# Optimization experiments

Hardware: AMD Instinct MI355X
Metric: run time of the kernel (lower is better)

The kernel has to match this reference:

```python
import jax, jax.numpy as jnp
import numpy as np

DIM = 512
GLBL = 108
N = 100000
NUM_SEGMENTS = 1024


def setup_inputs() -> dict:
    key = jax.random.key(0)
    ks = jax.random.split(key, 9)
    x = jax.random.normal(ks[0], (N, DIM), dtype=jnp.float32)
    glbl_x = jax.random.normal(ks[1], (N, GLBL), dtype=jnp.float32)
    batch = jnp.sort(jax.random.randint(ks[2], (N,), 0, NUM_SEGMENTS, dtype=jnp.int32))
    # MLP params: (dim+108 -> dim), (dim -> dim), (dim -> 1)
    s0 = 1.0 / np.sqrt(DIM + GLBL)
    s1 = 1.0 / np.sqrt(DIM)
    W0 = jax.random.uniform(ks[3], (DIM + GLBL, DIM), jnp.float32, -s0, s0)
    b0 = jax.random.uniform(ks[4], (DIM,), jnp.float32, -s0, s0)
    W1 = jax.random.uniform(ks[5], (DIM, DIM), jnp.float32, -s1, s1)
    b1 = jax.random.uniform(ks[6], (DIM,), jnp.float32, -s1, s1)
    W2 = jax.random.uniform(ks[7], (DIM, 1), jnp.float32, -s1, s1)
    b2 = jax.random.uniform(ks[8], (1,), jnp.float32, -s1, s1)
    return {"x": x, "batch": batch, "glbl_x": glbl_x,
            "W0": W0, "b0": b0, "W1": W1, "b1": b1, "W2": W2, "b2": b2}


def segment_softmax(logits, seg, num_segments):
    # logits: [N, 1]; per-segment numerically-stable softmax (torch_geometric softmax)
    m = jax.ops.segment_max(logits, seg, num_segments=num_segments)  # [G, 1]
    e = jnp.exp(logits - m[seg])
    s = jax.ops.segment_sum(e, seg, num_segments=num_segments)       # [G, 1]
    return e / (s[seg] + 1e-16)


def reference(x, batch, glbl_x, W0, b0, W1, b1, W2, b2):
    out = jnp.concatenate([x, glbl_x], axis=-1)          # [N, dim+108]
    out = jax.nn.softplus(out @ W0 + b0)                 # [N, dim]
    out = jax.nn.softplus(out @ W1 + b1)                 # [N, dim]
    out = out @ W2 + b2                                  # [N, 1]
    return segment_softmax(out, batch, NUM_SEGMENTS)     # [N, 1]
```

## Files before the change

kernel.cpp:

```cpp
#include <hip/hip_runtime.h>
#include <hip/hip_bf16.h>
#include <math.h>


#define NSEG 1024

typedef __attribute__((ext_vector_type(8))) short short8;
typedef __attribute__((ext_vector_type(4))) float f32x4;

__device__ __forceinline__ unsigned short f2bf(float f) {
  __hip_bfloat16 h = __float2bfloat16(f);
  return *reinterpret_cast<unsigned short*>(&h);
}
__device__ __forceinline__ float softplus_fast(float z) {
  float t = __expf(-fabsf(z));
  return fmaxf(z, 0.f) + __logf(1.f + t);
}
__device__ __forceinline__ void gll16(const void* g, void* l) {
  __builtin_amdgcn_global_load_lds(
      (const __attribute__((address_space(1))) void*)g,
      (__attribute__((address_space(3))) void*)l, 16, 0, 0);
}
__device__ __forceinline__ int xcd_swz(int bid, int nwg) {
  int q = nwg >> 3, r = nwg & 7, x = bid & 7, i = bid >> 3;
  return (x < r ? x * (q + 1) : r * (q + 1) + (x - r) * q) + i;
}

__global__ __launch_bounds__(256) void prep(const float* __restrict__ W0,
                                            const float* __restrict__ W1,
                                            unsigned short* __restrict__ W0T,
                                            unsigned short* __restrict__ W1T,
                                            float* __restrict__ logits, int Mp) {
  int t = blockIdx.x * 256 + threadIdx.x;
  if (t < 512 * 640) {
    int n = t / 640, k = t % 640;
    W0T[t] = f2bf(k < 620 ? W0[(size_t)k * 512 + n] : 0.f);
    return;
  }
  t -= 512 * 640;
  if (t < 512 * 512) {
    int n = t / 512, k = t % 512;
    W1T[t] = f2bf(W1[(size_t)k * 512 + n]);
    return;
  }
  t -= 512 * 512;
  if (t < Mp) logits[t] = 0.f;
}

__global__ __launch_bounds__(256) void pack_g(const float* __restrict__ gx,
                                              float* __restrict__ G32,
                                              int N, int Mp) {
  int t = blockIdx.x * 256 + threadIdx.x;
  if (t >= Mp * 32) return;
  int row = t >> 5, c = (t & 31) << 2;
  float4 v;
  v.x = (row < N && c + 0 < 108) ? gx[(size_t)row * 108 + c + 0] : 0.f;
  v.y = (row < N && c + 1 < 108) ? gx[(size_t)row * 108 + c + 1] : 0.f;
  v.z = (row < N && c + 2 < 108) ? gx[(size_t)row * 108 + c + 2] : 0.f;
  v.w = (row < N && c + 3 < 108) ? gx[(size_t)row * 108 + c + 3] : 0.f;
  *reinterpret_cast<float4*>(G32 + (size_t)row * 128 + c) = v;
}

__global__ __launch_bounds__(256, 3) void gemm0(const float* __restrict__ x,
                                                const float* __restrict__ G32,
                                                const unsigned short* __restrict__ W0T,
                                                const float* __restrict__ b0,
                                                unsigned short* __restrict__ H0,
                                                int N, int nwg) {
  constexpr int K = 640, KT = 20;
  __shared__ float Asf[2][128 * 32];
  __shared__ unsigned short Ws[2][128 * 32];
  const int L = xcd_swz(blockIdx.x, nwg);
  const int nt = L & 3, mt = L >> 2;
  const int tid = threadIdx.x, lane = tid & 63, wid = tid >> 6;
  const int wm = wid >> 1, wn = wid & 1, lm = lane & 15, rch = lane >> 4;

  const unsigned short* Wg = W0T + (size_t)(nt * 128) * K;

  f32x4 acc[4][4] = {};

  auto stageA = [&](int buf, int kb) {
#pragma unroll
    for (int i2 = 0; i2 < 4; ++i2) {
      int f = i2 * 256 + tid;
      int r = f >> 3, s = f & 7;
      int g4 = (s ^ (r & 7)) << 2;
      const float* src;
      if (kb < 512) {
        int rg = mt * 128 + r; if (rg >= N) rg = N - 1;
        src = x + (size_t)rg * 512 + kb + g4;
      } else {
        int rg = mt * 128 + r;
        src = G32 + (size_t)rg * 128 + (kb - 512) + g4;
      }
      gll16(src, &Asf[buf][r * 32 + s * 4]);
    }
  };
  auto stageW = [&](int buf, int kb) {
#pragma unroll
    for (int i2 = 0; i2 < 2; ++i2) {
      int f = i2 * 256 + tid;
      int row = f >> 2;
      int sc = ((f & 3) ^ ((row >> 1) & 3)) << 3;
      gll16(Wg + (size_t)row * K + kb + sc, &Ws[buf][f * 8]);
    }
  };

  stageA(0, 0);
  stageW(0, 0);

  for (int kt = 0; kt < KT; ++kt) {
    const int cur = kt & 1;
    __syncthreads();
    if (kt + 1 < KT) { stageA(cur ^ 1, (kt + 1) * 32); stageW(cur ^ 1, (kt + 1) * 32); }

    short8 af[4], wf[4];
#pragma unroll
    for (int mi = 0; mi < 4; ++mi) {
      int rw = wm * 64 + mi * 16 + lm;
      const float* base = &Asf[cur][rw * 32];
      f32x4 lo = *reinterpret_cast<const f32x4*>(base + ((((2 * rch) ^ (rw & 7)) << 2)));
      f32x4 hi = *reinterpret_cast<const f32x4*>(base + ((((2 * rch + 1) ^ (rw & 7)) << 2)));
      union { unsigned short u[8]; short8 s8; } cv;
#pragma unroll
      for (int j = 0; j < 4; ++j) { cv.u[j] = f2bf(lo[j]); cv.u[4 + j] = f2bf(hi[j]); }
      af[mi] = cv.s8;
    }
#pragma unroll
    for (int ni = 0; ni < 4; ++ni) {
      int rw = wn * 64 + ni * 16 + lm;
      wf[ni] = *reinterpret_cast<const short8*>(
          &Ws[cur][rw * 32 + ((rch ^ ((rw >> 1) & 3)) << 3)]);
    }
    __builtin_amdgcn_s_setprio(1);
#pragma unroll
    for (int mi = 0; mi < 4; ++mi)
#pragma unroll
      for (int ni = 0; ni < 4; ++ni)
        acc[mi][ni] = __builtin_amdgcn_mfma_f32_16x16x32_bf16(wf[ni], af[mi], acc[mi][ni], 0, 0, 0);
    __builtin_amdgcn_s_setprio(0);
  }

#pragma unroll
  for (int mi = 0; mi < 4; ++mi) {
    const int m = mt * 128 + wm * 64 + mi * 16 + lm;
#pragma unroll
    for (int ni = 0; ni < 4; ++ni) {
      const int n0 = nt * 128 + wn * 64 + ni * 16 + (rch << 2);
      const f32x4 bb = *reinterpret_cast<const f32x4*>(b0 + n0);
      f32x4 v = acc[mi][ni];
      union { unsigned short u[4]; uint2 qv; } o;
#pragma unroll
      for (int rr = 0; rr < 4; ++rr) o.u[rr] = f2bf(softplus_fast(v[rr] + bb[rr]));
      *reinterpret_cast<uint2*>(H0 + (size_t)m * 512 + n0) = o.qv;
    }
  }
}

__global__ __launch_bounds__(256, 4) void gemm1(const unsigned short* __restrict__ H0,
                                                const unsigned short* __restrict__ W1T,
                                                const float* __restrict__ b1,
                                                const float* __restrict__ W2,
                                                float* __restrict__ logits, int nwg) {
  constexpr int K = 512, KT = 16;
  __shared__ unsigned short As[2][128 * 32];
  __shared__ unsigned short Ws[2][128 * 32];
  const int L = xcd_swz(blockIdx.x, nwg);
  const int nt = L & 3, mt = L >> 2;
  const int tid = threadIdx.x, lane = tid & 63, wid = tid >> 6;
  const int wm = wid >> 1, wn = wid & 1, lm = lane & 15, rch = lane >> 4;

  const unsigned short* Ag = H0 + (size_t)(mt * 128) * K;
  const unsigned short* Wg = W1T + (size_t)(nt * 128) * K;

  f32x4 acc[4][4] = {};

  auto stage = [&](int buf, int kb) {
#pragma unroll
    for (int i2 = 0; i2 < 2; ++i2) {
      int f = i2 * 256 + tid;
      int row = f >> 2;
      int sc = ((f & 3) ^ ((row >> 1) & 3)) << 3;
      gll16(Ag + (size_t)row * K + kb + sc, &As[buf][f * 8]);
      gll16(Wg + (size_t)row * K + kb + sc, &Ws[buf][f * 8]);
    }
  };

  stage(0, 0);

  for (int kt = 0; kt < KT; ++kt) {
    const int cur = kt & 1;
    __syncthreads();
    if (kt + 1 < KT) stage(cur ^ 1, (kt + 1) * 32);

    short8 af[4], wf[4];
#pragma unroll
    for (int mi = 0; mi < 4; ++mi) {
      int rw = wm * 64 + mi * 16 + lm;
      af[mi] = *reinterpret_cast<const short8*>(
          &As[cur][rw * 32 + ((rch ^ ((rw >> 1) & 3)) << 3)]);
    }
#pragma unroll
    for (int ni = 0; ni < 4; ++ni) {
      int rw = wn * 64 + ni * 16 + lm;
      wf[ni] = *reinterpret_cast<const short8*>(
          &Ws[cur][rw * 32 + ((rch ^ ((rw >> 1) & 3)) << 3)]);
    }
    __builtin_amdgcn_s_setprio(1);
#pragma unroll
    for (int mi = 0; mi < 4; ++mi)
#pragma unroll
      for (int ni = 0; ni < 4; ++ni)
        acc[mi][ni] = __builtin_amdgcn_mfma_f32_16x16x32_bf16(wf[ni], af[mi], acc[mi][ni], 0, 0, 0);
    __builtin_amdgcn_s_setprio(0);
  }

#pragma unroll
  for (int mi = 0; mi < 4; ++mi) {
    const int m = mt * 128 + wm * 64 + mi * 16 + lm;
    float part = 0.f;
#pragma unroll
    for (int ni = 0; ni < 4; ++ni) {
      const int n0 = nt * 128 + wn * 64 + ni * 16 + (rch << 2);
      const f32x4 bb = *reinterpret_cast<const f32x4*>(b1 + n0);
      const f32x4 wv = *reinterpret_cast<const f32x4*>(W2 + n0);
      f32x4 v = acc[mi][ni];
#pragma unroll
      for (int rr = 0; rr < 4; ++rr) part += softplus_fast(v[rr] + bb[rr]) * wv[rr];
    }
    part += __shfl_xor(part, 16);
    part += __shfl_xor(part, 32);
    if (lane < 16) atomicAdd(logits + m, part);
  }
}

__global__ __launch_bounds__(256) void segsoftmax(const float* __restrict__ logits,
                                                  const int* __restrict__ batch,
                                                  float* __restrict__ out, int N) {
  const int g = blockIdx.x;
  const int tid = threadIdx.x;
  int lo = 0, hi = N;
  while (lo < hi) { int mid = (lo + hi) >> 1; if (batch[mid] < g) lo = mid + 1; else hi = mid; }
  const int beg = lo;
  hi = N;
  while (lo < hi) { int mid = (lo + hi) >> 1; if (batch[mid] < g + 1) lo = mid + 1; else hi = mid; }
  const int end = lo;
  if (beg >= end) return;

  __shared__ float sh[4];
  float m = -INFINITY;
  for (int i = beg + tid; i < end; i += 256) m = fmaxf(m, logits[i]);
#pragma unroll
  for (int o = 32; o; o >>= 1) m = fmaxf(m, __shfl_down(m, o));
  if ((tid & 63) == 0) sh[tid >> 6] = m;
  __syncthreads();
  m = fmaxf(fmaxf(sh[0], sh[1]), fmaxf(sh[2], sh[3]));
  __syncthreads();

  float s = 0.f;
  for (int i = beg + tid; i < end; i += 256) s += expf(logits[i] - m);
#pragma unroll
  for (int o = 32; o; o >>= 1) s += __shfl_down(s, o);
  if ((tid & 63) == 0) sh[tid >> 6] = s;
  __syncthreads();
  s = sh[0] + sh[1] + sh[2] + sh[3];

  const float inv = 1.f / (s + 1e-16f);
  for (int i = beg + tid; i < end; i += 256) out[i] = expf(logits[i] - m) * inv;
}

extern "C" void kernel_launch(void* const* d_in, const int* in_sizes, int n_in,
                              void* d_out, int out_size, void* d_ws, size_t ws_size,
                              hipStream_t stream) {
  const float* x = (const float*)d_in[0];
  const int* batch = (const int*)d_in[1];
  const float* gx = (const float*)d_in[2];
  const float* W0 = (const float*)d_in[3];
  const float* b0 = (const float*)d_in[4];
  const float* W1 = (const float*)d_in[5];
  const float* b1 = (const float*)d_in[6];
  const float* W2 = (const float*)d_in[7];
  float* out = (float*)d_out;

  const int N = in_sizes[1];
  const int Mp = ((N + 127) / 128) * 128;
  const int nwg = (Mp / 128) * 4;

  auto align256 = [](size_t v) { return (v + 255) & ~(size_t)255; };
  char* ws = (char*)d_ws;
  size_t off = 0;
  float* G32 = (float*)(ws + off);                   off = align256(off + (size_t)Mp * 128 * 4);
  unsigned short* W0T = (unsigned short*)(ws + off); off = align256(off + (size_t)512 * 640 * 2);
  unsigned short* W1T = (unsigned short*)(ws + off); off = align256(off + (size_t)512 * 512 * 2);
  unsigned short* H0 = (unsigned short*)(ws + off);  off = align256(off + (size_t)Mp * 512 * 2);
  float* logits = (float*)(ws + off);                off = align256(off + (size_t)Mp * 4);
  (void)ws_size; (void)n_in; (void)out_size;

  const int prep_elems = 512 * 640 + 512 * 512 + Mp;
  prep<<<(prep_elems + 255) / 256, 256, 0, stream>>>(W0, W1, W0T, W1T, logits, Mp);
  pack_g<<<(Mp * 32 + 255) / 256, 256, 0, stream>>>(gx, G32, N, Mp);

  gemm0<<<nwg, 256, 0, stream>>>(x, G32, W0T, b0, H0, N, nwg);
  gemm1<<<nwg, 256, 0, stream>>>(H0, W1T, b1, W2, logits, nwg);

  segsoftmax<<<NSEG, 256, 0, stream>>>(logits, batch, out, N);
}
```

Measured before the change: 273.2 us.

## Load gemm0 A operand directly to registers with two-stage prefetch

The fp32 A tile (x and padded glbl) is no longer staged through LDS. Each lane now loads its MFMA fragment rows straight into registers, two k-steps ahead, while W stays in LDS with a 4-deep ring buffer. A manual vmcnt wait and sched barriers order the loads around the MFMAs. This removes LDS traffic and bank pressure for the large fp32 A tile, but raises register use, so the occupancy hint drops from 3 to 2 blocks. Each lane's direct global loads are also less coalesced than the old staged loads.

Result: slower. 422.4 us (+54.7%).

```diff
diff --git a/kernel.cpp b/kernel.cpp
--- a/kernel.cpp
+++ b/kernel.cpp
@@ -61,15 +61,14 @@
   *reinterpret_cast<float4*>(G32 + (size_t)row * 128 + c) = v;
 }
 
-__global__ __launch_bounds__(256, 3) void gemm0(const float* __restrict__ x,
+__global__ __launch_bounds__(256, 2) void gemm0(const float* __restrict__ x,
                                                 const float* __restrict__ G32,
                                                 const unsigned short* __restrict__ W0T,
                                                 const float* __restrict__ b0,
                                                 unsigned short* __restrict__ H0,
                                                 int N, int nwg) {
   constexpr int K = 640, KT = 20;
-  __shared__ float Asf[2][128 * 32];
-  __shared__ unsigned short Ws[2][128 * 32];
+  __shared__ unsigned short Ws[4][128 * 32];
   const int L = xcd_swz(blockIdx.x, nwg);
   const int nt = L & 3, mt = L >> 2;
   const int tid = threadIdx.x, lane = tid & 63, wid = tid >> 6;
@@ -77,60 +76,70 @@
 
   const unsigned short* Wg = W0T + (size_t)(nt * 128) * K;
 
+  const float* rx[4];
+  const float* rg[4];
+#pragma unroll
+  for (int mi = 0; mi < 4; ++mi) {
+    int rgl = mt * 128 + wm * 64 + mi * 16 + lm;
+    int rc = rgl < N ? rgl : N - 1;
+    rx[mi] = x + (size_t)rc * 512 + rch * 8;
+    rg[mi] = G32 + (size_t)rgl * 128 + rch * 8;
+  }
+
   f32x4 acc[4][4] = {};
-
-  auto stageA = [&](int buf, int kb) {
-#pragma unroll
-    for (int i2 = 0; i2 < 4; ++i2) {
-      int f = i2 * 256 + tid;
-      int r = f >> 3, s = f & 7;
-      int g4 = (s ^ (r & 7)) << 2;
-      const float* src;
-      if (kb < 512) {
-        int rg = mt * 128 + r; if (rg >= N) rg = N - 1;
-        src = x + (size_t)rg * 512 + kb + g4;
-      } else {
-        int rg = mt * 128 + r;
-        src = G32 + (size_t)rg * 128 + (kb - 512) + g4;
-      }
-      gll16(src, &Asf[buf][r * 32 + s * 4]);
-    }
-  };
-  auto stageW = [&](int buf, int kb) {
+  f32x4 aA[8], aB[8];
+
+  auto issueW = [&](int kt2) {
 #pragma unroll
     for (int i2 = 0; i2 < 2; ++i2) {
       int f = i2 * 256 + tid;
       int row = f >> 2;
       int sc = ((f & 3) ^ ((row >> 1) & 3)) << 3;
-      gll16(Wg + (size_t)row * K + kb + sc, &Ws[buf][f * 8]);
+      gll16(Wg + (size_t)row * K + kt2 * 32 + sc, &Ws[kt2 & 3][f * 8]);
     }
   };
-
-  stageA(0, 0);
-  stageW(0, 0);
-
-  for (int kt = 0; kt < KT; ++kt) {
-    const int cur = kt & 1;
-    __syncthreads();
-    if (kt + 1 < KT) { stageA(cur ^ 1, (kt + 1) * 32); stageW(cur ^ 1, (kt + 1) * 32); }
-
-    short8 af[4], wf[4];
+  auto issueA = [&](int kt2, f32x4* aR) {
+    const int kb = kt2 * 32;
+    if (kb < 512) {
+#pragma unroll
+      for (int mi = 0; mi < 4; ++mi) {
+        aR[mi * 2 + 0] = *reinterpret_cast<const f32x4*>(rx[mi] + kb);
+        aR[mi * 2 + 1] = *reinterpret_cast<const f32x4*>(rx[mi] + kb + 4);
+      }
+    } else {
+#pragma unroll
+      for (int mi = 0; mi < 4; ++mi) {
+        aR[mi * 2 + 0] = *reinterpret_cast<const f32x4*>(rg[mi] + (kb - 512));
+        aR[mi * 2 + 1] = *reinterpret_cast<const f32x4*>(rg[mi] + (kb - 512) + 4);
+      }
+    }
+  };
+
+  auto body = [&](int kt, f32x4* aCur) {
+    __builtin_amdgcn_sched_barrier(0);
+    __builtin_amdgcn_s_barrier();
+    asm volatile("s_waitcnt vmcnt(18)" ::: "memory");
+    __builtin_amdgcn_sched_barrier(0);
+    if (kt + 2 < KT) issueW(kt + 2);
+    short8 af[4];
 #pragma unroll
     for (int mi = 0; mi < 4; ++mi) {
-      int rw = wm * 64 + mi * 16 + lm;
-      const float* base = &Asf[cur][rw * 32];
-      f32x4 lo = *reinterpret_cast<const f32x4*>(base + ((((2 * rch) ^ (rw & 7)) << 2)));
-      f32x4 hi = *reinterpret_cast<const f32x4*>(base + ((((2 * rch + 1) ^ (rw & 7)) << 2)));
       union { unsigned short u[8]; short8 s8; } cv;
 #pragma unroll
-      for (int j = 0; j < 4; ++j) { cv.u[j] = f2bf(lo[j]); cv.u[4 + j] = f2bf(hi[j]); }
+      for (int j = 0; j < 4; ++j) {
+        cv.u[j] = f2bf(aCur[mi * 2 + 0][j]);
+        cv.u[4 + j] = f2bf(aCur[mi * 2 + 1][j]);
+      }
       af[mi] = cv.s8;
     }
+    if (kt + 2 < KT) issueA(kt + 2, aCur);
+    __builtin_amdgcn_sched_barrier(0);
+    short8 wf[4];
 #pragma unroll
     for (int ni = 0; ni < 4; ++ni) {
       int rw = wn * 64 + ni * 16 + lm;
       wf[ni] = *reinterpret_cast<const short8*>(
-          &Ws[cur][rw * 32 + ((rch ^ ((rw >> 1) & 3)) << 3)]);
+          &Ws[kt & 3][rw * 32 + ((rch ^ ((rw >> 1) & 3)) << 3)]);
     }
     __builtin_amdgcn_s_setprio(1);
 #pragma unroll
@@ -139,6 +148,16 @@
       for (int ni = 0; ni < 4; ++ni)
         acc[mi][ni] = __builtin_amdgcn_mfma_f32_16x16x32_bf16(wf[ni], af[mi], acc[mi][ni], 0, 0, 0);
     __builtin_amdgcn_s_setprio(0);
+  };
+
+  issueW(0);
+  issueW(1);
+  issueA(0, aA);
+  issueA(1, aB);
+
+  for (int kt = 0; kt < KT; kt += 2) {
+    body(kt, aA);
+    body(kt + 1, aB);
   }
 
 #pragma unroll
```
